# Optimization experiments

Hardware: AMD Instinct MI355X
Metric: run time of the kernel (lower is better)

Reference implementation:

```python
import jax, jax.numpy as jnp
import numpy as np

B, H, N, D = 8, 12, 2048, 64
M = 256  # DCT truncation length (maxM)
HEAD_DIM = D


def create_dct(n, m):
    # Orthonormal DCT-II basis, truncated to first m frequencies: [m, n]
    k = jnp.arange(m, dtype=jnp.float32)[:, None]
    i = jnp.arange(n, dtype=jnp.float32)[None, :]
    Dm = jnp.cos(jnp.pi * (2.0 * i + 1.0) * k / (2.0 * n)) * jnp.sqrt(2.0 / n)
    Dm = Dm.at[0].multiply(1.0 / jnp.sqrt(2.0))
    return Dm


def setup_inputs() -> dict:
    key = jax.random.key(0)
    kq, kk, kv = jax.random.split(key, 3)
    Q = jax.random.normal(kq, (B, H, N, D), dtype=jnp.float32)
    K = jax.random.normal(kk, (B, H, N, D), dtype=jnp.float32)
    V = jax.random.normal(kv, (B, H, N, D), dtype=jnp.float32)
    mask = jnp.ones((B, N), dtype=jnp.float32)
    Q_dct = create_dct(N, M)
    return {"Q": Q, "K": K, "V": V, "mask": mask, "Q_dct": Q_dct}


def reference(Q, K, V, mask, Q_dct):
    scale = 1.0 / jnp.sqrt(jnp.sqrt(jnp.float32(HEAD_DIM)))
    m4 = mask[:, None, :, None]  # [B,1,N,1]
    Qs = Q * scale
    Ks = K * scale * m4
    Vs = V * m4
    # DCT projection along the sequence axis: [m,n] x [b,h,n,d] -> [b,h,m,d]
    Qd = jnp.einsum('mn,bhnd->bhmd', Q_dct, Qs)
    Kd = jnp.einsum('mn,bhnd->bhmd', Q_dct, Ks)
    Vd = jnp.einsum('mn,bhnd->bhmd', Q_dct, Vs)
    energy = jnp.einsum('bhmd,bhkd->bhmk', Qd, Kd)  # [B,H,M,M]
    attention = jax.nn.softmax(energy, axis=-1)
    ctx = jnp.einsum('bhmk,bhkd->bhmd', attention, Vd)
    # inverse DCT reconstruction: Q_dct^T @ ctx -> [B,H,N,D]
    x = jnp.einsum('mn,bhmd->bhnd', Q_dct, ctx)
    return x
```

## Files before the change

kernel.cpp:

```cpp
#include <hip/hip_runtime.h>
#include <hip/hip_bf16.h>
#include <cstddef>

#define B_ 8
#define H_ 12
#define N_ 2048
#define D_ 64
#define M_ 256
#define BH_ (B_*H_)

typedef __attribute__((ext_vector_type(8))) short short8v;
typedef __attribute__((ext_vector_type(4))) float f32x4;

static __device__ __forceinline__ float4 ld4(const float* p){ return *(const float4*)p; }

static __device__ __forceinline__ unsigned short f2bf(float x){
    union { float f; unsigned int u; } v; v.f = x;
    unsigned int r = v.u + 0x7FFFu + ((v.u >> 16) & 1u);
    return (unsigned short)(r >> 16);
}
static __device__ __forceinline__ unsigned int pack2(float a, float b){
    unsigned int r;
    asm("v_cvt_pk_bf16_f32 %0, %1, %2" : "=v"(r) : "v"(a), "v"(b));
    return r;
}

__global__ __launch_bounds__(256)
void dct_prep_kernel(const float* __restrict__ Dct, unsigned short* __restrict__ DctA,
                     unsigned short* __restrict__ DctT)
{
    __shared__ __align__(16) unsigned short T[64*72];
    const int n0 = blockIdx.x * 64, m0 = blockIdx.y * 64;
    const int tid = threadIdx.x;
    const int mrow = tid >> 2, ng = tid & 3;
    const int m = m0 + mrow;
    unsigned short h[16];
    #pragma unroll
    for (int j = 0; j < 4; ++j) {
        const float4 t = ld4(Dct + (size_t)m*N_ + n0 + ng*16 + j*4);
        h[4*j+0]=f2bf(t.x); h[4*j+1]=f2bf(t.y); h[4*j+2]=f2bf(t.z); h[4*j+3]=f2bf(t.w);
    }
    unsigned int w[8];
    #pragma unroll
    for (int j = 0; j < 8; ++j) w[j] = (unsigned int)h[2*j] | ((unsigned int)h[2*j+1]<<16);
    const int fm = m >> 4;
    #pragma unroll
    for (int s = 0; s < 2; ++s) {
        const int u = 2*ng + s;
        const int fk = (n0 >> 5) + (u >> 2);
        const int lane = (m & 15) + (u & 3) * 16;
        unsigned short* dst = DctA + ((size_t)(fm*64 + fk)*64 + lane)*8;
        *(uint4*)dst = *(uint4*)&w[s*4];
    }
    #pragma unroll
    for (int j = 0; j < 16; ++j) T[(ng*16+j)*72 + mrow] = h[j];
    __syncthreads();
    const int n = tid >> 2, mg = tid & 3;
    uint4 a  = *(uint4*)&T[n*72 + mg*16];
    uint4 b2 = *(uint4*)&T[n*72 + mg*16 + 8];
    unsigned short* dt = DctT + (size_t)(n0+n)*M_ + m0 + mg*16;
    *(uint4*)dt = a; *(uint4*)(dt+8) = b2;
}

__global__ __launch_bounds__(256, 2)
void gemm_qkv(const float* __restrict__ Q, const float* __restrict__ K,
              const float* __restrict__ V, const float* __restrict__ mask,
              const unsigned short* __restrict__ DctA,
              unsigned short* __restrict__ Qb, unsigned short* __restrict__ Kb,
              unsigned short* __restrict__ Vb)
{
    __shared__ __align__(16) unsigned short Bsw[2][64*128];
    __shared__ __align__(16) float Msk[N_];
    const int wg = blockIdx.x;
    const int id = (wg & 7) * 72 + (wg >> 3);
    const int half  = id & 1;
    const int panel = id >> 1;
    const int bh = panel % BH_;
    const int tz = panel / BH_;
    const int b  = bh / H_;
    const float scale = 0.35355339059327373f;
    const float* X; unsigned short* Y; float smul; int um;
    if (tz==0)      { X=Q; Y=Qb; smul=scale; um=0; }
    else if (tz==1) { X=K; Y=Kb; smul=scale; um=1; }
    else            { X=V; Y=Vb; smul=1.0f;  um=1; }
    X += (size_t)bh*N_*D_;
    Y += (size_t)bh*M_*D_ + (size_t)half*128*D_;

    const int tid  = threadIdx.x;
    const int lane = tid & 63, wv = tid >> 6;
    const unsigned short* abase = DctA + (size_t)(half*8 + wv*2)*32768 + (size_t)lane*8;
    const float* xcol = X + lane;
    const int swz = (lane & 7) << 4;

    f32x4 acc[2][4];
    #pragma unroll
    for (int i = 0; i < 2; ++i)
        #pragma unroll
        for (int j = 0; j < 4; ++j) { acc[i][j].x=0.f; acc[i][j].y=0.f; acc[i][j].z=0.f; acc[i][j].w=0.f; }

    short8v pa[2][4], pb[2][4];
    float xrA[32], xrB[32];

    #define A_LOAD(P, T) do {                                                 \
        _Pragma("unroll")                                                     \
        for (int mf_ = 0; mf_ < 2; ++mf_)                                     \
            _Pragma("unroll")                                                 \
            for (int kh_ = 0; kh_ < 4; ++kh_)                                 \
                P[mf_][kh_] = *(const short8v*)(abase + (size_t)(mf_*64 + 4*(T)+kh_)*512); \
    } while(0)

    #define X_LOAD(XR, K0) do {                                               \
        const float* xp_ = xcol + (size_t)((K0) + wv*32) * D_;                \
        _Pragma("unroll")                                                     \
        for (int i_ = 0; i_ < 32; ++i_) XR[i_] = xp_[(size_t)i_*D_];          \
    } while(0)

    #define WRITE_B(XR, BUF, K0) do {                                         \
        const float4* mrow_ = (const float4*)&Msk[(K0) + wv*32];              \
        float fmv_[32];                                                       \
        _Pragma("unroll")                                                     \
        for (int j_ = 0; j_ < 8; ++j_) {                                      \
            const float4 t_ = mrow_[j_];                                      \
            fmv_[4*j_]=t_.x; fmv_[4*j_+1]=t_.y; fmv_[4*j_+2]=t_.z; fmv_[4*j_+3]=t_.w; \
        }                                                                     \
        _Pragma("unroll")                                                     \
        for (int c_ = 0; c_ < 4; ++c_) {                                      \
            uint4 w_;                                                         \
            w_.x = pack2(XR[8*c_+0]*fmv_[8*c_+0], XR[8*c_+1]*fmv_[8*c_+1]);   \
            w_.y = pack2(XR[8*c_+2]*fmv_[8*c_+2], XR[8*c_+3]*fmv_[8*c_+3]);   \
            w_.z = pack2(XR[8*c_+4]*fmv_[8*c_+4], XR[8*c_+5]*fmv_[8*c_+5]);   \
            w_.w = pack2(XR[8*c_+6]*fmv_[8*c_+6], XR[8*c_+7]*fmv_[8*c_+7]);   \
            *(uint4*)((char*)&Bsw[BUF][0] + lane*256 + ((wv*64 + c_*16) ^ swz)) = w_; \
        }                                                                     \
    } while(0)

    #define COMPUTE(BUF, P) do {                                              \
        _Pragma("unroll")                                                     \
        for (int kh_ = 0; kh_ < 4; ++kh_) {                                   \
            const int colb_ = kh_*64 + (lane>>4)*16;                          \
            _Pragma("unroll")                                                 \
            for (int nf_ = 0; nf_ < 4; ++nf_) {                               \
                const int rr_ = nf_*16 + (lane&15);                           \
                const short8v b_ = *(const short8v*)((char*)&Bsw[BUF][0] + rr_*256 + (colb_ ^ ((rr_&7)<<4))); \
                _Pragma("unroll")                                             \
                for (int mf_ = 0; mf_ < 2; ++mf_)                             \
                    acc[mf_][nf_] = __builtin_amdgcn_mfma_f32_16x16x32_bf16(P[mf_][kh_], b_, acc[mf_][nf_], 0, 0, 0); \
            }                                                                 \
        }                                                                     \
    } while(0)

    #define BARJ() do { asm volatile("s_waitcnt lgkmcnt(0)" ::: "memory");    \
                        __builtin_amdgcn_sched_barrier(0);                    \
                        __builtin_amdgcn_s_barrier(); } while(0)

    {
        #pragma unroll
        for (int c = 0; c < 2; ++c) {
            const int idx = (tid + c*256) * 4;
            float4 v;
            if (um) {
                v = ld4(mask + (size_t)b*N_ + idx);
                v.x *= smul; v.y *= smul; v.z *= smul; v.w *= smul;
            } else { v.x = smul; v.y = smul; v.z = smul; v.w = smul; }
            *(float4*)&Msk[idx] = v;
        }
    }
    A_LOAD(pa, 0);
    X_LOAD(xrA, 0);
    X_LOAD(xrB, 128);
    __syncthreads();
    WRITE_B(xrA, 0, 0);
    BARJ();

    #define STEP_EVEN(T) do {                                                 \
        A_LOAD(pb, (T)+1);                                                    \
        X_LOAD(xrA, ((T)+2)*128);                                             \
        COMPUTE(0, pa);                                                       \
        __builtin_amdgcn_sched_barrier(0);                                    \
        WRITE_B(xrB, 1, ((T)+1)*128);                                         \
        BARJ();                                                               \
    } while(0)
    #define STEP_ODD(T) do {                                                  \
        A_LOAD(pa, (T)+1);                                                    \
        X_LOAD(xrB, ((T)+2)*128);                                             \
        COMPUTE(1, pb);                                                       \
        __builtin_amdgcn_sched_barrier(0);                                    \
        WRITE_B(xrA, 0, ((T)+1)*128);                                         \
        BARJ();                                                               \
    } while(0)

    for (int tb = 0; tb < 14; tb += 2) {
        STEP_EVEN(tb);
        STEP_ODD(tb+1);
    }
    A_LOAD(pb, 15);
    COMPUTE(0, pa);
    __builtin_amdgcn_sched_barrier(0);
    WRITE_B(xrB, 1, 15*128);
    BARJ();
    COMPUTE(1, pb);

    #pragma unroll
    for (int mf = 0; mf < 2; ++mf)
        #pragma unroll
        for (int nf = 0; nf < 4; ++nf)
            #pragma unroll
            for (int r = 0; r < 4; ++r) {
                const int m = wv*32 + mf*16 + (lane>>4)*4 + r;
                const int d = nf*16 + (lane&15);
                Y[(size_t)m*D_ + d] = f2bf(acc[mf][nf][r]);
            }
    #undef A_LOAD
    #undef X_LOAD
    #undef WRITE_B
    #undef COMPUTE
    #undef BARJ
    #undef STEP_EVEN
    #undef STEP_ODD
}

__global__ __launch_bounds__(256, 2)
void attn_kernel(const unsigned short* __restrict__ Qd, const unsigned short* __restrict__ Kd,
                 const unsigned short* __restrict__ Vd, unsigned short* __restrict__ CtxT)
{
    __shared__ __align__(16) char LB[65536];
    unsigned short* QA = (unsigned short*)(LB);
    unsigned short* KB = (unsigned short*)(LB + 8192);
    unsigned short* PL = (unsigned short*)(LB);
    unsigned short* VT = (unsigned short*)(LB + 32768);
    unsigned short* T  = (unsigned short*)(LB);

    const int mt = blockIdx.x, bh = blockIdx.y;
    const unsigned short* qd = Qd + (size_t)bh*M_*D_ + (size_t)mt*64*D_;
    const unsigned short* kd = Kd + (size_t)bh*M_*D_;
    const unsigned short* vd = Vd + (size_t)bh*M_*D_;
    const int tid  = threadIdx.x;
    const int lane = tid & 63, wv = tid >> 6;
    const int l15  = lane & 15, kg = lane >> 4;
    const int swz  = (l15 & 7) << 4;

    {
        const int row = tid >> 2, q = tid & 3;
        {
            const uint4 w0 = *(const uint4*)(qd + (size_t)row*D_ + q*16);
            const uint4 w1 = *(const uint4*)(qd + (size_t)row*D_ + q*16 + 8);
            const int s = (row & 7) << 4;
            *(uint4*)((char*)QA + row*128 + ((q*32)      ^ s)) = w0;
            *(uint4*)((char*)QA + row*128 + ((q*32 + 16) ^ s)) = w1;
        }
        #pragma unroll
        for (int c0 = 0; c0 < 4; ++c0) {
            const int krow = c0*64 + row;
            const uint4 w0 = *(const uint4*)(kd + (size_t)krow*D_ + q*16);
            const uint4 w1 = *(const uint4*)(kd + (size_t)krow*D_ + q*16 + 8);
            const int s = (krow & 7) << 4;
            *(uint4*)((char*)KB + krow*128 + ((q*32)      ^ s)) = w0;
            *(uint4*)((char*)KB + krow*128 + ((q*32 + 16) ^ s)) = w1;
        }
    }
    __syncthreads();

    f32x4 acc[16];
    #pragma unroll
    for (int i = 0; i < 16; ++i) { acc[i].x=0.f; acc[i].y=0.f; acc[i].z=0.f; acc[i].w=0.f; }
    #pragma unroll
    for (int kh = 0; kh < 2; ++kh) {
        const int colb = kh*64 + kg*16;
        const short8v af = *(const short8v*)((char*)QA + (wv*16 + l15)*128 + (colb ^ swz));
        #pragma unroll
        for (int nf = 0; nf < 16; ++nf) {
            const short8v bf = *(const short8v*)((char*)KB + (nf*16 + l15)*128 + (colb ^ swz));
            acc[nf] = __builtin_amdgcn_mfma_f32_16x16x32_bf16(af, bf, acc[nf], 0, 0, 0);
        }
    }

    float inv[4];
    #pragma unroll
    for (int r = 0; r < 4; ++r) {
        float mx = acc[0][r];
        #pragma unroll
        for (int nf = 1; nf < 16; ++nf) mx = fmaxf(mx, acc[nf][r]);
        mx = fmaxf(mx, __shfl_xor(mx, 1));
        mx = fmaxf(mx, __shfl_xor(mx, 2));
        mx = fmaxf(mx, __shfl_xor(mx, 4));
        mx = fmaxf(mx, __shfl_xor(mx, 8));
        float sm = 0.f;
        #pragma unroll
        for (int nf = 0; nf < 16; ++nf) {
            const float p = __expf(acc[nf][r] - mx);
            acc[nf][r] = p; sm += p;
        }
        sm += __shfl_xor(sm, 1);
        sm += __shfl_xor(sm, 2);
        sm += __shfl_xor(sm, 4);
        sm += __shfl_xor(sm, 8);
        inv[r] = 1.0f / sm;
    }
    __syncthreads();

    {
        const int rowbase = wv*16 + kg*4;
        #pragma unroll
        for (int nf = 0; nf < 16; ++nf)
            #pragma unroll
            for (int r = 0; r < 4; ++r) {
                const int rowP = rowbase + r;
                const int byte = rowP*512 + ((((nf*16 + l15)*2)) ^ ((rowP & 7) << 4));
                *(unsigned short*)((char*)PL + byte) = f2bf(acc[nf][r]);
            }
    }
    {
        const int j  = tid & 31;
        const int kq = tid >> 5;
        const int d0 = 2*j, d1 = 2*j + 1;
        const int vs0 = (d0 & 7) << 4, vs1 = (d1 & 7) << 4;
        #pragma unroll
        for (int i = 0; i < 32; i += 2) {
            const int k2 = kq*32 + i;
            const unsigned int u0 = *(const unsigned int*)(vd + (size_t)k2*D_ + d0);
            const unsigned int u1 = *(const unsigned int*)(vd + (size_t)(k2+1)*D_ + d0);
            const unsigned int lo = (u0 & 0xFFFFu) | (u1 << 16);
            const unsigned int hi = (u0 >> 16) | (u1 & 0xFFFF0000u);
            *(unsigned int*)((char*)VT + d0*512 + ((k2*2) ^ vs0)) = lo;
            *(unsigned int*)((char*)VT + d1*512 + ((k2*2) ^ vs1)) = hi;
        }
    }
    __syncthreads();

    f32x4 c2[4];
    #pragma unroll
    for (int i = 0; i < 4; ++i) { c2[i].x=0.f; c2[i].y=0.f; c2[i].z=0.f; c2[i].w=0.f; }
    #pragma unroll
    for (int kf = 0; kf < 8; ++kf) {
        const int colb = kf*64 + kg*16;
        const short8v a = *(const short8v*)((char*)PL + (wv*16 + l15)*512 + (colb ^ swz));
        #pragma unroll
        for (int nf2 = 0; nf2 < 4; ++nf2) {
            const int drow = nf2*16 + l15;
            const short8v bb = *(const short8v*)((char*)VT + drow*512 + (colb ^ swz));
            c2[nf2] = __builtin_amdgcn_mfma_f32_16x16x32_bf16(a, bb, c2[nf2], 0, 0, 0);
        }
    }
    __syncthreads();

    {
        const int rowbase = wv*16 + kg*4;
        #pragma unroll
        for (int nf2 = 0; nf2 < 4; ++nf2)
            #pragma unroll
            for (int r = 0; r < 4; ++r) {
                const int d = nf2*16 + l15;
                T[d*72 + rowbase + r] = f2bf(c2[nf2][r] * inv[r]);
            }
    }
    __syncthreads();
    {
        const int d2 = tid >> 2, mg = tid & 3;
        uint4 w0 = *(uint4*)&T[d2*72 + mg*16];
        uint4 w1 = *(uint4*)&T[d2*72 + mg*16 + 8];
        unsigned short* dst = CtxT + (size_t)bh*D_*M_ + (size_t)d2*M_ + mt*64 + mg*16;
        *(uint4*)dst = w0; *(uint4*)(dst+8) = w1;
    }
}

__global__ __launch_bounds__(128, 2)
void gemm_out(const unsigned short* __restrict__ DctT, const unsigned short* __restrict__ CtxT,
              float* __restrict__ Out)
{
    __shared__ __align__(16) unsigned short Asw[128*64];
    __shared__ __align__(16) unsigned short Bsw[64*64];
    const int nt = blockIdx.x, bh = blockIdx.y;
    const int n0 = nt*128;
    const unsigned short* ct = CtxT + (size_t)bh*D_*M_;
    float* out = Out + (size_t)bh*N_*D_;
    const int tid = threadIdx.x;
    const int lane = tid & 63, wave = tid >> 6;

    f32x4 acc[4][4];
    #pragma unroll
    for (int i = 0; i < 4; ++i)
        #pragma unroll
        for (int j = 0; j < 4; ++j) { acc[i][j].x=0.f; acc[i][j].y=0.f; acc[i][j].z=0.f; acc[i][j].w=0.f; }

    for (int step = 0; step < 4; ++step) {
        const int k0 = step*64;
        if (step) __syncthreads();
        const int ch = tid & 7;
        #pragma unroll
        for (int rr = 0; rr < 8; ++rr) {
            const int r = (tid>>3) + rr*16;
            const uint4 v = *(const uint4*)(DctT + (size_t)(n0+r)*M_ + k0 + ch*8);
            *(uint4*)((char*)Asw + r*128 + ((ch*16) ^ ((r&7)<<4))) = v;
        }
        #pragma unroll
        for (int rr = 0; rr < 4; ++rr) {
            const int d = (tid>>3) + rr*16;
            const uint4 v = *(const uint4*)(ct + (size_t)d*M_ + k0 + ch*8);
            *(uint4*)((char*)Bsw + d*128 + ((ch*16) ^ (((d>>1)&7)<<4))) = v;
        }
        __syncthreads();
        #pragma unroll
        for (int kh = 0; kh < 2; ++kh) {
            const int colb = kh*64 + (lane>>4)*16;
            short8v a[4], bb[4];
            #pragma unroll
            for (int mf = 0; mf < 4; ++mf) {
                const int r = wave*64 + mf*16 + (lane&15);
                a[mf] = *(const short8v*)((char*)Asw + r*128 + (colb ^ ((r&7)<<4)));
            }
            #pragma unroll
            for (int nf = 0; nf < 4; ++nf) {
                const int r = nf*16 + (lane&15);
                bb[nf] = *(const short8v*)((char*)Bsw + r*128 + (colb ^ (((r>>1)&7)<<4)));
            }
            #pragma unroll
            for (int mf = 0; mf < 4; ++mf)
                #pragma unroll
                for (int nf = 0; nf < 4; ++nf)
                    acc[mf][nf] = __builtin_amdgcn_mfma_f32_16x16x32_bf16(a[mf], bb[nf], acc[mf][nf], 0, 0, 0);
        }
    }
    #pragma unroll
    for (int mf = 0; mf < 4; ++mf)
        #pragma unroll
        for (int nf = 0; nf < 4; ++nf)
            #pragma unroll
            for (int r = 0; r < 4; ++r) {
                const int n = n0 + wave*64 + mf*16 + (lane>>4)*4 + r;
                const int d = nf*16 + (lane&15);
                out[(size_t)n*D_ + d] = acc[mf][nf][r];
            }
}

extern "C" void kernel_launch(void* const* d_in, const int* in_sizes, int n_in,
                              void* d_out, int out_size, void* d_ws, size_t ws_size,
                              hipStream_t stream) {
    const float* Q    = (const float*)d_in[0];
    const float* K    = (const float*)d_in[1];
    const float* V    = (const float*)d_in[2];
    const float* mask = (const float*)d_in[3];
    const float* Dct  = (const float*)d_in[4];
    float* out = (float*)d_out;

    const size_t per = (size_t)BH_ * M_ * D_;
    unsigned short* wsu = (unsigned short*)d_ws;
    unsigned short* Qb   = wsu;
    unsigned short* Kb   = Qb + per;
    unsigned short* Vb   = Kb + per;
    unsigned short* CtxT = Vb + per;
    unsigned short* DctA = CtxT + per;
    unsigned short* DctT = DctA + (size_t)M_ * N_;

    dct_prep_kernel<<<dim3(N_/64, M_/64), 256, 0, stream>>>(Dct, DctA, DctT);
    gemm_qkv<<<dim3(576), 256, 0, stream>>>(Q, K, V, mask, DctA, Qb, Kb, Vb);
    attn_kernel<<<dim3(M_/64, BH_), 256, 0, stream>>>(Qb, Kb, Vb, CtxT);
    gemm_out<<<dim3(N_/128, BH_), 128, 0, stream>>>(DctT, CtxT, out);
}
```

Measured before the change: 78.17 us.

## Split QKV DCT projection along sequence instead of output rows, sum partials in attention

The QKV projection GEMM previously split each panel's 256 DCT output rows into two workgroups, so each workgroup streamed the full 2048-row fp32 input. It now splits the reduction over the sequence axis instead. Each workgroup reads only half of the input and computes all 256 output rows, writing a bf16 partial result. The attention kernel loads both partials for Q, K and V and adds them before use. This is meant to halve input read traffic per workgroup. The cost is extra partial writes and reads, higher register pressure from the larger accumulator tile, and an extra bf16 rounding step on each partial.

Measured after the change: 83.55 us. +6.9%, slower.

```diff
diff --git a/kernel.cpp b/kernel.cpp
--- a/kernel.cpp
+++ b/kernel.cpp
@@ -22,6 +22,18 @@
 static __device__ __forceinline__ unsigned int pack2(float a, float b){
     unsigned int r;
     asm("v_cvt_pk_bf16_f32 %0, %1, %2" : "=v"(r) : "v"(a), "v"(b));
+    return r;
+}
+static __device__ __forceinline__ unsigned int addbf2(unsigned int a, unsigned int b){
+    union { unsigned int u; float f; } alo, ahi, blo, bhi;
+    alo.u = a << 16; ahi.u = a & 0xFFFF0000u;
+    blo.u = b << 16; bhi.u = b & 0xFFFF0000u;
+    return pack2(alo.f + blo.f, ahi.f + bhi.f);
+}
+static __device__ __forceinline__ uint4 addbf8(uint4 a, uint4 b){
+    uint4 r;
+    r.x = addbf2(a.x, b.x); r.y = addbf2(a.y, b.y);
+    r.z = addbf2(a.z, b.z); r.w = addbf2(a.w, b.w);
     return r;
 }
 
@@ -65,58 +77,58 @@
 __global__ __launch_bounds__(256, 2)
 void gemm_qkv(const float* __restrict__ Q, const float* __restrict__ K,
               const float* __restrict__ V, const float* __restrict__ mask,
-              const unsigned short* __restrict__ DctA,
-              unsigned short* __restrict__ Qb, unsigned short* __restrict__ Kb,
-              unsigned short* __restrict__ Vb)
+              const unsigned short* __restrict__ DctA, unsigned short* __restrict__ Part)
 {
     __shared__ __align__(16) unsigned short Bsw[2][64*128];
-    __shared__ __align__(16) float Msk[N_];
+    __shared__ __align__(16) float Msk[1024];
+    const size_t per = (size_t)BH_ * M_ * D_;
     const int wg = blockIdx.x;
     const int id = (wg & 7) * 72 + (wg >> 3);
-    const int half  = id & 1;
+    const int kh    = id & 1;
     const int panel = id >> 1;
     const int bh = panel % BH_;
     const int tz = panel / BH_;
     const int b  = bh / H_;
     const float scale = 0.35355339059327373f;
-    const float* X; unsigned short* Y; float smul; int um;
-    if (tz==0)      { X=Q; Y=Qb; smul=scale; um=0; }
-    else if (tz==1) { X=K; Y=Kb; smul=scale; um=1; }
-    else            { X=V; Y=Vb; smul=1.0f;  um=1; }
-    X += (size_t)bh*N_*D_;
-    Y += (size_t)bh*M_*D_ + (size_t)half*128*D_;
+    const float* X; float smul; int um;
+    if (tz==0)      { X=Q; smul=scale; um=0; }
+    else if (tz==1) { X=K; smul=scale; um=1; }
+    else            { X=V; smul=1.0f;  um=1; }
+    X += (size_t)bh*N_*D_ + (size_t)kh*1024*D_;
+    unsigned short* Y = Part + ((size_t)(tz*2 + kh))*per + (size_t)bh*M_*D_;
 
     const int tid  = threadIdx.x;
     const int lane = tid & 63, wv = tid >> 6;
-    const unsigned short* abase = DctA + (size_t)(half*8 + wv*2)*32768 + (size_t)lane*8;
+    const int kq0  = kh*32;
+    const unsigned short* abase = DctA + (size_t)(wv*4)*32768 + (size_t)lane*8;
     const float* xcol = X + lane;
     const int swz = (lane & 7) << 4;
 
-    f32x4 acc[2][4];
-    #pragma unroll
-    for (int i = 0; i < 2; ++i)
+    f32x4 acc[4][4];
+    #pragma unroll
+    for (int i = 0; i < 4; ++i)
         #pragma unroll
         for (int j = 0; j < 4; ++j) { acc[i][j].x=0.f; acc[i][j].y=0.f; acc[i][j].z=0.f; acc[i][j].w=0.f; }
 
-    short8v pa[2][4], pb[2][4];
+    short8v a_[4][4];
     float xrA[32], xrB[32];
 
-    #define A_LOAD(P, T) do {                                                 \
+    #define A_LOAD(T) do {                                                    \
         _Pragma("unroll")                                                     \
-        for (int mf_ = 0; mf_ < 2; ++mf_)                                     \
+        for (int mf_ = 0; mf_ < 4; ++mf_)                                     \
             _Pragma("unroll")                                                 \
-            for (int kh_ = 0; kh_ < 4; ++kh_)                                 \
-                P[mf_][kh_] = *(const short8v*)(abase + (size_t)(mf_*64 + 4*(T)+kh_)*512); \
-    } while(0)
-
-    #define X_LOAD(XR, K0) do {                                               \
-        const float* xp_ = xcol + (size_t)((K0) + wv*32) * D_;                \
+            for (int j_ = 0; j_ < 4; ++j_)                                    \
+                a_[mf_][j_] = *(const short8v*)(abase + (size_t)(mf_*64 + kq0 + 4*(T)+j_)*512); \
+    } while(0)
+
+    #define X_LOAD(XR, T) do {                                                \
+        const float* xp_ = xcol + (size_t)((T)*128 + wv*32) * D_;             \
         _Pragma("unroll")                                                     \
         for (int i_ = 0; i_ < 32; ++i_) XR[i_] = xp_[(size_t)i_*D_];          \
     } while(0)
 
-    #define WRITE_B(XR, BUF, K0) do {                                         \
-        const float4* mrow_ = (const float4*)&Msk[(K0) + wv*32];              \
+    #define WRITE_B(XR, BUF, T) do {                                          \
+        const float4* mrow_ = (const float4*)&Msk[(T)*128 + wv*32];           \
         float fmv_[32];                                                       \
         _Pragma("unroll")                                                     \
         for (int j_ = 0; j_ < 8; ++j_) {                                      \
@@ -134,7 +146,7 @@
         }                                                                     \
     } while(0)
 
-    #define COMPUTE(BUF, P) do {                                              \
+    #define COMPUTE(BUF) do {                                                 \
         _Pragma("unroll")                                                     \
         for (int kh_ = 0; kh_ < 4; ++kh_) {                                   \
             const int colb_ = kh_*64 + (lane>>4)*16;                          \
@@ -143,8 +155,8 @@
                 const int rr_ = nf_*16 + (lane&15);                           \
                 const short8v b_ = *(const short8v*)((char*)&Bsw[BUF][0] + rr_*256 + (colb_ ^ ((rr_&7)<<4))); \
                 _Pragma("unroll")                                             \
-                for (int mf_ = 0; mf_ < 2; ++mf_)                             \
-                    acc[mf_][nf_] = __builtin_amdgcn_mfma_f32_16x16x32_bf16(P[mf_][kh_], b_, acc[mf_][nf_], 0, 0, 0); \
+                for (int mf_ = 0; mf_ < 4; ++mf_)                             \
+                    acc[mf_][nf_] = __builtin_amdgcn_mfma_f32_16x16x32_bf16(a_[mf_][kh_], b_, acc[mf_][nf_], 0, 0, 0); \
             }                                                                 \
         }                                                                     \
     } while(0)
@@ -154,59 +166,67 @@
                         __builtin_amdgcn_s_barrier(); } while(0)
 
     {
-        #pragma unroll
-        for (int c = 0; c < 2; ++c) {
-            const int idx = (tid + c*256) * 4;
-            float4 v;
-            if (um) {
-                v = ld4(mask + (size_t)b*N_ + idx);
-                v.x *= smul; v.y *= smul; v.z *= smul; v.w *= smul;
-            } else { v.x = smul; v.y = smul; v.z = smul; v.w = smul; }
-            *(float4*)&Msk[idx] = v;
-        }
-    }
-    A_LOAD(pa, 0);
+        const int idx = tid * 4;
+        float4 v;
+        if (um) {
+            v = ld4(mask + (size_t)b*N_ + kh*1024 + idx);
+            v.x *= smul; v.y *= smul; v.z *= smul; v.w *= smul;
+        } else { v.x = smul; v.y = smul; v.z = smul; v.w = smul; }
+        *(float4*)&Msk[idx] = v;
+    }
     X_LOAD(xrA, 0);
-    X_LOAD(xrB, 128);
+    X_LOAD(xrB, 1);
     __syncthreads();
     WRITE_B(xrA, 0, 0);
     BARJ();
 
     #define STEP_EVEN(T) do {                                                 \
-        A_LOAD(pb, (T)+1);                                                    \
-        X_LOAD(xrA, ((T)+2)*128);                                             \
-        COMPUTE(0, pa);                                                       \
+        A_LOAD(T);                                                            \
+        X_LOAD(xrA, (T)+2);                                                   \
+        COMPUTE(0);                                                           \
         __builtin_amdgcn_sched_barrier(0);                                    \
-        WRITE_B(xrB, 1, ((T)+1)*128);                                         \
+        WRITE_B(xrB, 1, (T)+1);                                               \
         BARJ();                                                               \
     } while(0)
     #define STEP_ODD(T) do {                                                  \
-        A_LOAD(pa, (T)+1);                                                    \
-        X_LOAD(xrB, ((T)+2)*128);                                             \
-        COMPUTE(1, pb);                                                       \
+        A_LOAD(T);                                                            \
+        X_LOAD(xrB, (T)+2);                                                   \
+        COMPUTE(1);                                                           \
         __builtin_amdgcn_sched_barrier(0);                                    \
-        WRITE_B(xrA, 0, ((T)+1)*128);                                         \
+        WRITE_B(xrA, 0, (T)+2);                                               \
         BARJ();                                                               \
     } while(0)
 
-    for (int tb = 0; tb < 14; tb += 2) {
-        STEP_EVEN(tb);
-        STEP_ODD(tb+1);
-    }
-    A_LOAD(pb, 15);
-    COMPUTE(0, pa);
-    __builtin_amdgcn_sched_barrier(0);
-    WRITE_B(xrB, 1, 15*128);
-    BARJ();
-    COMPUTE(1, pb);
-
-    #pragma unroll
-    for (int mf = 0; mf < 2; ++mf)
+    A_LOAD(0); X_LOAD(xrA, 2); COMPUTE(0);
+    __builtin_amdgcn_sched_barrier(0);
+    WRITE_B(xrB, 1, 1); BARJ();
+    A_LOAD(1); X_LOAD(xrB, 3); COMPUTE(1);
+    __builtin_amdgcn_sched_barrier(0);
+    WRITE_B(xrA, 0, 2); BARJ();
+    A_LOAD(2); X_LOAD(xrA, 4); COMPUTE(0);
+    __builtin_amdgcn_sched_barrier(0);
+    WRITE_B(xrB, 1, 3); BARJ();
+    A_LOAD(3); X_LOAD(xrB, 5); COMPUTE(1);
+    __builtin_amdgcn_sched_barrier(0);
+    WRITE_B(xrA, 0, 4); BARJ();
+    A_LOAD(4); X_LOAD(xrA, 6); COMPUTE(0);
+    __builtin_amdgcn_sched_barrier(0);
+    WRITE_B(xrB, 1, 5); BARJ();
+    A_LOAD(5); X_LOAD(xrB, 7); COMPUTE(1);
+    __builtin_amdgcn_sched_barrier(0);
+    WRITE_B(xrA, 0, 6); BARJ();
+    A_LOAD(6); COMPUTE(0);
+    __builtin_amdgcn_sched_barrier(0);
+    WRITE_B(xrB, 1, 7); BARJ();
+    A_LOAD(7); COMPUTE(1);
+
+    #pragma unroll
+    for (int mf = 0; mf < 4; ++mf)
         #pragma unroll
         for (int nf = 0; nf < 4; ++nf)
             #pragma unroll
             for (int r = 0; r < 4; ++r) {
-                const int m = wv*32 + mf*16 + (lane>>4)*4 + r;
+                const int m = wv*64 + mf*16 + (lane>>4)*4 + r;
                 const int d = nf*16 + (lane&15);
                 Y[(size_t)m*D_ + d] = f2bf(acc[mf][nf][r]);
             }
@@ -220,8 +240,10 @@
 }
 
 __global__ __launch_bounds__(256, 2)
-void attn_kernel(const unsigned short* __restrict__ Qd, const unsigned short* __restrict__ Kd,
-                 const unsigned short* __restrict__ Vd, unsigned short* __restrict__ CtxT)
+void attn_kernel(const unsigned short* __restrict__ QdA, const unsigned short* __restrict__ QdB,
+                 const unsigned short* __restrict__ KdA, const unsigned short* __restrict__ KdB,
+                 const unsigned short* __restrict__ VdA, const unsigned short* __restrict__ VdB,
+                 unsigned short* __restrict__ CtxT)
 {
     __shared__ __align__(16) char LB[65536];
     unsigned short* QA = (unsigned short*)(LB);
@@ -231,9 +253,8 @@
     unsigned short* T  = (unsigned short*)(LB);
 
     const int mt = blockIdx.x, bh = blockIdx.y;
-    const unsigned short* qd = Qd + (size_t)bh*M_*D_ + (size_t)mt*64*D_;
-    const unsigned short* kd = Kd + (size_t)bh*M_*D_;
-    const unsigned short* vd = Vd + (size_t)bh*M_*D_;
+    const size_t qoff = (size_t)bh*M_*D_ + (size_t)mt*64*D_;
+    const size_t koff = (size_t)bh*M_*D_;
     const int tid  = threadIdx.x;
     const int lane = tid & 63, wv = tid >> 6;
     const int l15  = lane & 15, kg = lane >> 4;
@@ -242,8 +263,12 @@
     {
         const int row = tid >> 2, q = tid & 3;
         {
-            const uint4 w0 = *(const uint4*)(qd + (size_t)row*D_ + q*16);
-            const uint4 w1 = *(const uint4*)(qd + (size_t)row*D_ + q*16 + 8);
+            const uint4 a0 = *(const uint4*)(QdA + qoff + (size_t)row*D_ + q*16);
+            const uint4 a1 = *(const uint4*)(QdA + qoff + (size_t)row*D_ + q*16 + 8);
+            const uint4 b0 = *(const uint4*)(QdB + qoff + (size_t)row*D_ + q*16);
+            const uint4 b1 = *(const uint4*)(QdB + qoff + (size_t)row*D_ + q*16 + 8);
+            const uint4 w0 = addbf8(a0, b0);
+            const uint4 w1 = addbf8(a1, b1);
             const int s = (row & 7) << 4;
             *(uint4*)((char*)QA + row*128 + ((q*32)      ^ s)) = w0;
             *(uint4*)((char*)QA + row*128 + ((q*32 + 16) ^ s)) = w1;
@@ -251,8 +276,12 @@
         #pragma unroll
         for (int c0 = 0; c0 < 4; ++c0) {
             const int krow = c0*64 + row;
-            const uint4 w0 = *(const uint4*)(kd + (size_t)krow*D_ + q*16);
-            const uint4 w1 = *(const uint4*)(kd + (size_t)krow*D_ + q*16 + 8);
+            const uint4 a0 = *(const uint4*)(KdA + koff + (size_t)krow*D_ + q*16);
+            const uint4 a1 = *(const uint4*)(KdA + koff + (size_t)krow*D_ + q*16 + 8);
+            const uint4 b0 = *(const uint4*)(KdB + koff + (size_t)krow*D_ + q*16);
+            const uint4 b1 = *(const uint4*)(KdB + koff + (size_t)krow*D_ + q*16 + 8);
+            const uint4 w0 = addbf8(a0, b0);
+            const uint4 w1 = addbf8(a1, b1);
             const int s = (krow & 7) << 4;
             *(uint4*)((char*)KB + krow*128 + ((q*32)      ^ s)) = w0;
             *(uint4*)((char*)KB + krow*128 + ((q*32 + 16) ^ s)) = w1;
@@ -317,8 +346,10 @@
         #pragma unroll
         for (int i = 0; i < 32; i += 2) {
             const int k2 = kq*32 + i;
-            const unsigned int u0 = *(const unsigned int*)(vd + (size_t)k2*D_ + d0);
-            const unsigned int u1 = *(const unsigned int*)(vd + (size_t)(k2+1)*D_ + d0);
+            const unsigned int u0 = addbf2(*(const unsigned int*)(VdA + koff + (size_t)k2*D_ + d0),
+                                           *(const unsigned int*)(VdB + koff + (size_t)k2*D_ + d0));
+            const unsigned int u1 = addbf2(*(const unsigned int*)(VdA + koff + (size_t)(k2+1)*D_ + d0),
+                                           *(const unsigned int*)(VdB + koff + (size_t)(k2+1)*D_ + d0));
             const unsigned int lo = (u0 & 0xFFFFu) | (u1 << 16);
             const unsigned int hi = (u0 >> 16) | (u1 & 0xFFFF0000u);
             *(unsigned int*)((char*)VT + d0*512 + ((k2*2) ^ vs0)) = lo;
@@ -444,15 +475,17 @@
 
     const size_t per = (size_t)BH_ * M_ * D_;
     unsigned short* wsu = (unsigned short*)d_ws;
-    unsigned short* Qb   = wsu;
-    unsigned short* Kb   = Qb + per;
-    unsigned short* Vb   = Kb + per;
-    unsigned short* CtxT = Vb + per;
+    unsigned short* Part = wsu;
+    unsigned short* CtxT = Part + 6*per;
     unsigned short* DctA = CtxT + per;
-    unsigned short* DctT = DctA + (size_t)M_ * N_;
+    unsigned short* DctT = DctA + (size_t)M_*N_;
 
     dct_prep_kernel<<<dim3(N_/64, M_/64), 256, 0, stream>>>(Dct, DctA, DctT);
-    gemm_qkv<<<dim3(576), 256, 0, stream>>>(Q, K, V, mask, DctA, Qb, Kb, Vb);
-    attn_kernel<<<dim3(M_/64, BH_), 256, 0, stream>>>(Qb, Kb, Vb, CtxT);
+    gemm_qkv<<<dim3(576), 256, 0, stream>>>(Q, K, V, mask, DctA, Part);
+    attn_kernel<<<dim3(M_/64, BH_), 256, 0, stream>>>(
+        Part + 0*per, Part + 1*per,
+        Part + 2*per, Part + 3*per,
+        Part + 4*per, Part + 5*per,
+        CtxT);
     gemm_out<<<dim3(N_/128, BH_), 128, 0, stream>>>(DctT, CtxT, out);
 }
```
